# Kernel optimization log

Hardware: AMD Instinct MI355X
Metric: run time of the kernel (lower is better)

## Reference

```python
import jax, jax.numpy as jnp
import numpy as np

N_SAMPLES = 32768; N_FRAMES = 128; MODEL_DIM = 128; N_EVENTS = 16
N_BANDS = 64; RESOLUTION = 32; SR = 22050.0; WINDOW = 512; STEP = 256
DILATIONS = [1, 3, 9, 27, 1]

def conv1d(x, w, b, dilation=1):
    # x (B,C,T), w (O,I,K), 'same' padding
    k = w.shape[-1]; total = dilation * (k - 1)
    pad = (total // 2, total - total // 2)
    y = jax.lax.conv_general_dilated(x, w, (1,), [pad], rhs_dilation=(dilation,),
                                     dimension_numbers=('NCH', 'OIH', 'NCH'))
    return y + b[None, :, None]

def conv_transpose1d(x, w, b):
    # torch ConvTranspose1d(k=4, s=2, p=1): doubles length
    y = jax.lax.conv_general_dilated(x, w[..., ::-1], (1,), [(2, 2)], lhs_dilation=(2,),
                                     dimension_numbers=('NCH', 'OIH', 'NCH'))
    return y + b[None, :, None]

def example_norm(x):
    n = jnp.sqrt(jnp.sum(x * x, axis=(1, 2), keepdims=True))
    return x / (n + 1e-8)

def interp_linear(x, size):
    # F.interpolate(mode='linear', align_corners=False)
    T = x.shape[-1]
    c = jnp.clip((jnp.arange(size) + 0.5) * T / size - 0.5, 0.0, T - 1.0)
    i0 = jnp.floor(c).astype(jnp.int32)
    i1 = jnp.minimum(i0 + 1, T - 1)
    w = (c - i0).astype(x.dtype)
    return x[..., i0] * (1 - w) + x[..., i1] * w

def fft_convolve(a, b):
    n = a.shape[-1]
    pa = [(0, 0)] * (a.ndim - 1) + [(0, n)]
    pb = [(0, 0)] * (b.ndim - 1) + [(0, n)]
    spec = jnp.fft.rfft(jnp.pad(a, pa), norm='ortho') * jnp.fft.rfft(jnp.pad(b, pb), norm='ortho')
    return jnp.fft.irfft(spec, n=2 * n, norm='ortho')[..., :n]

def conv_up_nearest(z, lin_w, lin_b, up_w, up_b, out_w, out_b, start):
    h = (z @ lin_w.T + lin_b).reshape(-1, MODEL_DIM, start)
    for i in range(up_w.shape[0]):
        h = jnp.repeat(h, 2, axis=-1)
        h = jax.nn.leaky_relu(conv1d(h, up_w[i], up_b[i]), 0.2)
    return conv1d(h, out_w, out_b)

def conv_up_learned(z, lin_w, lin_b, up_w, up_b, out_w, out_b, start):
    h = (z @ lin_w.T + lin_b).reshape(-1, MODEL_DIM, start)
    for i in range(up_w.shape[0]):
        h = jax.nn.leaky_relu(conv_transpose1d(h, up_w[i], up_b[i]), 0.2)
    return conv1d(h, out_w, out_b)

def resonance_bank():
    # (n_bands, resolution, n_samples): per-band sinusoid * per-resolution frame-wise decay
    freqs = jnp.geomspace(20.0, SR * 0.45, N_BANDS)
    t = jnp.arange(N_SAMPLES, dtype=jnp.float32) / SR
    sines = jnp.sin(2.0 * np.pi * freqs[:, None] * t[None, :])
    decays = jnp.linspace(0.5, 0.9999, RESOLUTION)
    amp = decays[:, None] ** jnp.arange(N_FRAMES, dtype=jnp.float32)[None, :]
    amp = jnp.repeat(amp, N_SAMPLES // N_FRAMES, axis=-1)  # (res, N)
    return sines[:, None, :] * amp[None, :, :]

def _forward(x, noise, fb_w, reduce_w, reduce_b, dl_dw, dl_db, dl_pw, dl_pb,
             tt_w, tt_b, tr_w, tr_b,
             pos_lin_w, pos_lin_b, pos_up_w, pos_up_b, pos_out_w, pos_out_b,
             env_lin_w, env_lin_b, env_up_w, env_up_b, env_out_w, env_out_b,
             tfu_lin_w, tfu_lin_b, tfu_up_w, tfu_up_b, tfu_out_w, tfu_out_b):
    batch = x.shape[0]
    # filterbank conv + temporal pooling (avg pool 512/256) -> (B, 128, 128)
    h = jax.lax.conv_general_dilated(x, fb_w, (1,), [(256, 255)],
                                     dimension_numbers=('NCH', 'OIH', 'NCH'))
    h = jax.lax.reduce_window(h, 0.0, jax.lax.add, (1, 1, WINDOW), (1, 1, STEP),
                              [(0, 0), (0, 0), (STEP, STEP)]) / WINDOW
    h = example_norm(h[..., :N_FRAMES])
    # positional encoding: 1 + 16 sin + 16 cos = 33 channels
    p = jnp.linspace(-1.0, 1.0, N_FRAMES)
    bands = [p[None]]
    for i in range(16):
        f = p * (2.0 ** i) * np.pi
        bands.append(jnp.sin(f)[None]); bands.append(jnp.cos(f)[None])
    pos = jnp.broadcast_to(jnp.concatenate(bands, axis=0)[None], (batch, 33, N_FRAMES)).astype(x.dtype)
    h = jnp.concatenate([h, pos], axis=1)
    h = jnp.einsum('oc,bct->bot', reduce_w, h) + reduce_b[None, :, None]
    # dilated context stack with residuals
    for i, d in enumerate(DILATIONS):
        y = conv1d(h, dl_dw[i], dl_db[i], dilation=d)
        y = jnp.einsum('oc,bct->bot', dl_pw[i], y) + dl_pb[i][None, :, None]
        h = jax.nn.leaky_relu(h + y, 0.2)
    h = example_norm(h)
    # vectorwise top-k sparsity: keep 16 unit-normalized time-step vectors
    norms = jnp.sqrt(jnp.sum(h * h, axis=1))               # (B, T)
    hn = h / (norms[:, None, :] + 1e-8)
    _, idx = jax.lax.top_k(norms, N_EVENTS)                # (B, 16)
    encoded = jnp.take_along_axis(hn.transpose(0, 2, 1), idx[..., None], axis=1)  # (B,16,C)
    e = encoded.reshape(-1, MODEL_DIM)                     # (B*16, C)
    time = e @ tt_w.T + tt_b
    transfer = e @ tr_w.T + tr_b                           # VQ is passthrough
    # impulse placement: learned upsample -> softmax -> sparse comb
    pimp = conv_up_learned(time, pos_lin_w, pos_lin_b, pos_up_w, pos_up_b, pos_out_w, pos_out_b, 4).reshape(-1, 128)
    impulse = jnp.zeros((pimp.shape[0], N_SAMPLES), pimp.dtype).at[:, ::N_SAMPLES // 128].set(jax.nn.softmax(pimp, axis=-1))
    impulse = impulse.reshape(batch, N_EVENTS, N_SAMPLES)
    # segment generator: envelope * noise, transfer-function decode via FFT conv
    env = jax.nn.relu(conv_up_nearest(transfer, env_lin_w, env_lin_b, env_up_w, env_up_b, env_out_w, env_out_b, 4))  # (BE,1,256)
    orig_env = env
    envs = interp_linear(env, N_SAMPLES) * noise           # (BE,1,N)
    tfl = conv_up_nearest(transfer, tfu_lin_w, tfu_lin_b, tfu_up_w, tfu_up_b, tfu_out_w, tfu_out_b, 8)  # (BE,32,bands)
    tfl = tfl.transpose(0, 2, 1)                           # (BE,bands,res)
    sm = jax.nn.softmax(tfl, axis=-1)
    hard = jax.nn.one_hot(jnp.argmax(tfl, axis=-1), RESOLUTION, dtype=tfl.dtype)
    sel = sm + jax.lax.stop_gradient(hard - sm)            # straight-through hard select
    bank = resonance_bank().astype(x.dtype)
    tf_sig = jnp.einsum('ebr,brt->ebt', sel, bank)         # (BE,bands,N)
    final = jnp.mean(fft_convolve(envs, tf_sig), axis=1, keepdims=True)  # (BE,1,N)
    ev = fft_convolve(final.reshape(batch, N_EVENTS, N_SAMPLES), impulse)
    output = jnp.sum(ev, axis=1, keepdims=True)            # (B,1,N)
    return output, idx, encoded, orig_env.reshape(batch, N_EVENTS, -1), time, transfer

def setup_inputs() -> dict:
    key = jax.random.key(0)
    ks = jax.random.split(key, 32)
    r = lambda i, shape: jax.random.normal(ks[i], shape, dtype=jnp.float32) * 0.05
    B = 1
    return {
        'x': jax.random.normal(ks[0], (B, 1, N_SAMPLES), dtype=jnp.float32),
        'noise': jax.random.uniform(ks[1], (1, 1, N_SAMPLES), minval=-1.0, maxval=1.0, dtype=jnp.float32),
        'fb_w': r(2, (128, 1, 512)),
        'reduce_w': r(3, (128, 161)), 'reduce_b': r(4, (128,)),
        'dl_dw': r(5, (5, 128, 128, 3)), 'dl_db': r(6, (5, 128)),
        'dl_pw': r(7, (5, 128, 128)), 'dl_pb': r(8, (5, 128)),
        'tt_w': r(9, (128, 128)), 'tt_b': r(10, (128,)),
        'tr_w': r(11, (128, 128)), 'tr_b': r(12, (128,)),
        'pos_lin_w': r(13, (512, 128)), 'pos_lin_b': r(14, (512,)),
        'pos_up_w': r(15, (5, 128, 128, 4)), 'pos_up_b': r(16, (5, 128)),
        'pos_out_w': r(17, (1, 128, 3)), 'pos_out_b': r(18, (1,)),
        'env_lin_w': r(19, (512, 128)), 'env_lin_b': r(20, (512,)),
        'env_up_w': r(21, (6, 128, 128, 3)), 'env_up_b': r(22, (6, 128)),
        'env_out_w': r(23, (1, 128, 3)), 'env_out_b': r(24, (1,)),
        'tfu_lin_w': r(25, (1024, 128)), 'tfu_lin_b': r(26, (1024,)),
        'tfu_up_w': r(27, (3, 128, 128, 3)), 'tfu_up_b': r(28, (3, 128)),
        'tfu_out_w': r(29, (32, 128, 3)), 'tfu_out_b': r(30, (32,)),
    }

def reference(x, noise, fb_w, reduce_w, reduce_b, dl_dw, dl_db, dl_pw, dl_pb,
              tt_w, tt_b, tr_w, tr_b,
              pos_lin_w, pos_lin_b, pos_up_w, pos_up_b, pos_out_w, pos_out_b,
              env_lin_w, env_lin_b, env_up_w, env_up_b, env_out_w, env_out_b,
              tfu_lin_w, tfu_lin_b, tfu_up_w, tfu_up_b, tfu_out_w, tfu_out_b):
    return _forward(x, noise, fb_w, reduce_w, reduce_b, dl_dw, dl_db, dl_pw, dl_pb,
                    tt_w, tt_b, tr_w, tr_b,
                    pos_lin_w, pos_lin_b, pos_up_w, pos_up_b, pos_out_w, pos_out_b,
                    env_lin_w, env_lin_b, env_up_w, env_up_b, env_out_w, env_out_b,
                    tfu_lin_w, tfu_lin_b, tfu_up_w, tfu_up_b, tfu_out_w, tfu_out_b)
```

## Files before the change

kernel.cpp:

```cpp
#include <hip/hip_runtime.h>
#include <math.h>

#define NSAMP 32768
#define NFRM  128

static constexpr int S_OFF  = 0;
static constexpr int HP     = 32772;
static constexpr int NSQ    = HP + 16384;
static constexpr int HA     = NSQ + 16;
static constexpr int HB     = HA + 16384;
static constexpr int TFQ    = HA;
static constexpr int WC     = HB + 16384;
static constexpr int WBC    = WC + 245760;
static constexpr int EWS    = WBC + 640;
static constexpr int TIMEO  = EWS + 2048;
static constexpr int TRANSO = TIMEO + 2048;
static constexpr int PE     = TRANSO + 2048;
static constexpr int RSEL   = PE + 2048;
static constexpr int ENVO   = RSEL + 1024;
static constexpr int BUFA   = ENVO + 4096;
static constexpr int BUFB   = BUFA + 524288;
static constexpr int WT     = BUFB + 524288;
static constexpr int WT_POS = WT;
static constexpr int WT_ENV = WT + 327680;
static constexpr int WT_TFU = WT + 622592;
static constexpr int WT_TT  = WT + 770048;
static constexpr int WT_TR  = WT + 786432;
static constexpr int LT_POS = WT + 802816;
static constexpr int LT_ENV = WT + 868352;
static constexpr int LT_TFU = WT + 933888;
static constexpr int SINES  = WT + 1064960;
static constexpr int ENVS   = SINES + 2097152;
static constexpr int SLAB   = SINES;
static constexpr int CRB0   = ENVS + 524288;
static constexpr int CRB1   = CRB0 + 262656;
static constexpr int KB     = CRB1 + 262656;
static constexpr int PA     = KB + 278528;
static constexpr int PB     = PA + 262144;
static constexpr int TA     = PB + 262144;
static constexpr int TB     = TA + 131072;

static constexpr int O_IDX  = 32768;
static constexpr int O_ENC  = 32784;
static constexpr int O_ENV  = 34832;
static constexpr int O_TIME = 38928;
static constexpr int O_TR   = 40976;

typedef short bf16x8 __attribute__((ext_vector_type(8)));
typedef float f32x4  __attribute__((ext_vector_type(4)));
typedef float f32x16 __attribute__((ext_vector_type(16)));

static __device__ __forceinline__ unsigned short f2bf(float f){
  unsigned int u = __float_as_uint(f);
  unsigned int r = (u + 0x7FFFu + ((u >> 16) & 1u)) >> 16;
  return (unsigned short)r;
}

__global__ void k_setup(const float* __restrict__ x,
                        const float* __restrict__ posw, const float* __restrict__ envw,
                        const float* __restrict__ tfuw, const float* __restrict__ ttw,
                        const float* __restrict__ trw,  const float* __restrict__ lpw,
                        const float* __restrict__ lew,  const float* __restrict__ ltw,
                        const float* __restrict__ dw,   const float* __restrict__ db,
                        const float* __restrict__ pw,   const float* __restrict__ pb2,
                        float* __restrict__ ws){
  __shared__ float ps[1024];
  int b = blockIdx.x, tid = threadIdx.x;
  if (b == 0){
    float* S = ws + S_OFF;
    float v[32];
    const float4* x4 = (const float4*)(x + tid*32);
    float s = 0.f;
#pragma unroll
    for (int i=0;i<8;++i){
      float4 q = x4[i];
      v[4*i]=q.x; v[4*i+1]=q.y; v[4*i+2]=q.z; v[4*i+3]=q.w;
      s += q.x+q.y+q.z+q.w;
    }
    ps[tid] = s; __syncthreads();
    for (int ofs=1; ofs<1024; ofs<<=1){
      float add = (tid>=ofs)? ps[tid-ofs] : 0.f;
      __syncthreads();
      ps[tid] += add;
      __syncthreads();
    }
    float run = ps[tid] - s;
#pragma unroll
    for (int i=0;i<32;++i){ S[tid*32+i] = run; run += v[i]; }
    if (tid==1023) S[32768] = ps[1023];
  } else if (b < 1041){
    int i = (b-1)*1024 + tid;
    float v;
    if (i < 327680){
      int l = i>>16, r = i & 65535, o = r & 127, ck = r>>7, c = ck>>2, k = ck&3;
      v = posw[(l<<16) + (((o<<7)+c)<<2) + k];
    } else if (i < 622592){
      int i2 = i - 327680; int l = i2/49152, r = i2 - l*49152, o = r&127, ck = r>>7;
      int c = ck/3, k = ck - 3*c;
      v = envw[l*49152 + ((o<<7)+c)*3 + k];
    } else if (i < 770048){
      int i2 = i - 622592; int l = i2/49152, r = i2 - l*49152, o = r&127, ck = r>>7;
      int c = ck/3, k = ck - 3*c;
      v = tfuw[l*49152 + ((o<<7)+c)*3 + k];
    } else if (i < 786432){
      int i2 = i - 770048; int o = i2 & 127, c = i2 >> 7;
      v = ttw[(o<<7) + c];
    } else if (i < 802816){
      int i2 = i - 786432; int o = i2 & 127, c = i2 >> 7;
      v = trw[(o<<7) + c];
    } else if (i < 868352){
      int i2 = i - 802816; int s = i2 >> 14, k = (i2 >> 7) & 127, c = i2 & 127;
      v = lpw[(((c<<2)+s)<<7) + k];
    } else if (i < 933888){
      int i2 = i - 868352; int s = i2 >> 14, k = (i2 >> 7) & 127, c = i2 & 127;
      v = lew[(((c<<2)+s)<<7) + k];
    } else {
      int i2 = i - 933888; int s = i2 >> 14, k = (i2 >> 7) & 127, c = i2 & 127;
      v = ltw[(((c<<3)+s)<<7) + k];
    }
    ws[WT + i] = v;
  } else if (b < 1121){
    int idx = (b-1041)*1024 + tid;
    if (idx < 81920){
      int l = idx >> 14, r = idx & 16383, o = r >> 7, c = r & 127;
      float a0=0.f, a1=0.f, a2=0.f;
      for (int m=0;m<128;++m){
        float p = pw[(l*128 + o)*128 + m];
        const float* dp = dw + ((l*128 + m)*128 + c)*3;
        a0 += p*dp[0]; a1 += p*dp[1]; a2 += p*dp[2];
      }
      float* W = ws + WC + ((l*128 + o)*128 + c)*3;
      W[0]=a0; W[1]=a1; W[2]=a2;
      if (c==0){
        float bb = pb2[l*128 + o];
        for (int m=0;m<128;++m) bb += pw[(l*128 + o)*128 + m] * db[l*128 + m];
        ws[WBC + l*128 + o] = bb;
      }
    }
  } else if (b < 3169){
    int b2 = b - 1121;
    int band = b2 >> 5;
    int t = ((b2 & 31) << 10) + tid;
    if (tid == 0){
      float l0 = __fdiv_rn((float)log(20.0),   (float)log(10.0));
      float l1 = __fdiv_rn((float)log(9922.5), (float)log(10.0));
      float dl = __fdiv_rn(__fsub_rn(l1, l0), 63.0f);
      float lb = __fadd_rn(l0, __fmul_rn((float)band, dl));
      float freq = (float)pow(10.0, (double)lb);
      ps[0] = __fmul_rn((float)(2.0*M_PI), freq);
    }
    __syncthreads();
    float w = ps[0];
    float tn = __fdiv_rn((float)t, 22050.0f);
    ws[SINES + band*NSAMP + t] = sinf(__fmul_rn(w, tn));
  } else {
    int i = (b-3169)*1024 + tid;
    {
      int e = i >> 11, r = i & 2047;
      ((unsigned short*)(ws + KB))[e*34816 + r] = 0;
    }
    if (i < 16*128){
      int e = i >> 7, r = i & 127;
      if (r < 64) ((unsigned short*)(ws + CRB0))[e*32832 + (r==0 ? 0 : 32768 + r)] = 0;
      else        ((unsigned short*)(ws + CRB1))[e*32832 + 32768 + (r-64)] = 0;
    }
  }
}


__global__ void k_fbpool(const float* __restrict__ fbw, float* __restrict__ ws){
  const float* S = ws + S_OFF;
  int c = blockIdx.x >> 5, j0 = (blockIdx.x & 31) << 2;
  int jj = threadIdx.x >> 7, kk = threadIdx.x & 127;
  int j = j0 + jj;
  int i0 = max(0, 256*j - 256), i1 = min(32767, 256*j + 255);
  float acc = 0.f;
#pragma unroll
  for (int m=0;m<4;++m){
    int k = kk + (m<<7);
    int hi = min(max(i1 + k - 255, 0), 32768);
    int lo = min(max(i0 + k - 256, 0), 32768);
    acc += fbw[c*512 + k] * (S[hi] - S[lo]);
  }
  for (int o=32;o;o>>=1) acc += __shfl_down(acc, o);
  __shared__ float red[8];
  if ((threadIdx.x & 63) == 0) red[threadIdx.x>>6] = acc;
  __syncthreads();
  if (threadIdx.x < 4)
    ws[HP + c*128 + j0 + threadIdx.x] = (red[2*threadIdx.x] + red[2*threadIdx.x+1]) * (1.0f/512.0f);
}

__global__ void k_reduce(const float* __restrict__ rw, const float* __restrict__ rb,
                         float* __restrict__ ws){
  int o = blockIdx.x, t = threadIdx.x;
  const float* hp = ws + HP;
  float sq = 0.f;
  for (int i=t;i<16384;i+=128){ float v = hp[i]; sq += v*v; }
  for (int ofs=32;ofs;ofs>>=1) sq += __shfl_down(sq, ofs);
  __shared__ float rr2[2];
  if ((t & 63) == 0) rr2[t>>6] = sq;
  __syncthreads();
  float g = sqrtf(rr2[0] + rr2[1]) + 1e-8f;
  float acc = rb[o];
  for (int c=0;c<128;++c) acc += rw[o*161 + c] * __fdiv_rn(hp[c*128 + t], g);
  float delta = __fdiv_rn(2.0f, 127.0f);
  float p = __fadd_rn(-1.0f, __fmul_rn((float)t, delta));
  acc += rw[o*161 + 128] * p;
  float sc = 1.0f;
  const float PIF = (float)M_PI;
#pragma unroll
  for (int i=0;i<16;++i){
    float f = __fmul_rn(__fmul_rn(p, sc), PIF);
    acc += rw[o*161 + 129 + 2*i] * sinf(f);
    acc += rw[o*161 + 130 + 2*i] * cosf(f);
    sc = sc * 2.0f;
  }
  ws[HA + o*128 + t] = acc;
}

__global__ void k_dil(float* __restrict__ ws, int l, int d, int inoff, int outoff){
  __shared__ float xin[16384];
  __shared__ float pr[256];
  int o = blockIdx.x, tid = threadIdx.x;
  int t = tid & 127, half = tid >> 7;
  const float* in = ws + inoff;
  for (int idx=tid; idx<16384; idx+=256) xin[idx] = in[idx];
  __syncthreads();
  const float* Wo = ws + WC + (l*128 + o)*384 + half*192;
  float acc = (half == 0) ? (xin[o*128 + t] + ws[WBC + l*128 + o]) : 0.f;
  int cbase = half << 6;
  for (int c2=0;c2<64;++c2){
    int c = cbase + c2;
    float v0 = (t-d >= 0)  ? xin[c*128 + t - d] : 0.f;
    float v1 = xin[c*128 + t];
    float v2 = (t+d < 128) ? xin[c*128 + t + d] : 0.f;
    acc += Wo[c2*3]*v0 + Wo[c2*3+1]*v1 + Wo[c2*3+2]*v2;
  }
  pr[half*128 + t] = acc;
  __syncthreads();
  if (tid < 128){
    float a = pr[tid] + pr[128 + tid];
    ws[outoff + o*128 + tid] = a >= 0.f ? a : 0.2f*a;
  }
}

__global__ void k_topk(float* __restrict__ ws, float* __restrict__ out){
  const float* h = ws + HB;
  int tid = threadIdx.x;
  int g = tid >> 7, t = tid & 127;
  __shared__ float xs[16384];
  __shared__ float part[1024];
  __shared__ float nt[128], nt0[128], csh[128];
  __shared__ int idxs[16];
  __shared__ float gsh[1];
  __shared__ float wv[2]; __shared__ int wi[2];
  for (int idx=tid; idx<16384; idx+=1024){
    int c = idx >> 7, tt = idx & 127;
    xs[(c<<7) + ((tt+c)&127)] = h[idx];
  }
  __syncthreads();
  float p = 0.f;
  for (int c=g; c<128; c+=8){ float v = xs[(c<<7) + ((t+c)&127)]; p += v*v; }
  part[tid] = p;
  __syncthreads();
  if (tid < 128){
    float cs = 0.f;
#pragma unroll
    for (int gg=0; gg<8; ++gg) cs += part[(gg<<7) + tid];
    csh[tid] = cs;
  }
  __syncthreads();
  if (tid < 64){
    float s = csh[tid] + csh[tid+64];
    for (int o=32;o;o>>=1) s += __shfl_down(s, o);
    if (tid == 0) gsh[0] = sqrtf(s) + 1e-8f;
  }
  __syncthreads();
  float g2 = gsh[0];
  float p2 = 0.f;
  for (int c=g; c<128; c+=8){ float v = __fdiv_rn(xs[(c<<7) + ((t+c)&127)], g2); p2 += v*v; }
  part[tid] = p2;
  __syncthreads();
  if (tid < 128){
    float cs = 0.f;
#pragma unroll
    for (int gg=0; gg<8; ++gg) cs += part[(gg<<7) + tid];
    float ntv = sqrtf(cs);
    nt[tid] = ntv; nt0[tid] = ntv;
  }
  __syncthreads();
  for (int j=0;j<16;++j){
    if (tid < 128){
      float v = nt[t]; int bi = t;
      for (int o=32;o;o>>=1){
        float ov = __shfl_down(v, o); int oi = __shfl_down(bi, o);
        if (ov > v || (ov == v && oi < bi)){ v = ov; bi = oi; }
      }
      if ((t & 63) == 0){ wv[t>>6] = v; wi[t>>6] = bi; }
    }
    __syncthreads();
    if (tid == 0){
      int win = (wv[1] > wv[0] || (wv[1] == wv[0] && wi[1] < wi[0])) ? wi[1] : wi[0];
      idxs[j] = win; nt[win] = -3.0e38f;
    }
    __syncthreads();
  }
  if (tid < 16) out[O_IDX + tid] = (float)idxs[tid];
  for (int pos=tid; pos<2048; pos+=1024){
    int j = pos >> 7, ch = pos & 127;
    int ij = idxs[j];
    float hv = __fdiv_rn(xs[(ch<<7) + ((ij+ch)&127)], g2);
    float enc = __fdiv_rn(hv, nt0[ij] + 1e-8f);
    out[O_ENC + pos] = enc;
    ws[EWS + pos] = enc;
  }
}

__global__ void k_tt(float* __restrict__ ws, const float* __restrict__ ttb,
                     const float* __restrict__ trb, float* __restrict__ out){
  int kind = blockIdx.x >> 4, j = blockIdx.x & 15;
  int tid = threadIdx.x;
  int o = tid & 127, cg = tid >> 7;
  __shared__ float er[128];
  __shared__ float part[8][128];
  if (tid < 128) er[tid] = ws[EWS + j*128 + tid];
  __syncthreads();
  const float* Wt = ws + (kind ? WT_TR : WT_TT);
  float acc = 0.f;
  for (int c=cg; c<128; c+=8) acc += er[c] * Wt[c*128 + o];
  part[cg][o] = acc;
  __syncthreads();
  if (tid < 128){
    float a = kind ? trb[tid] : ttb[tid];
#pragma unroll
    for (int g=0; g<8; ++g) a += part[g][tid];
    out[(kind ? O_TR : O_TIME) + j*128 + tid] = a;
    ws[(kind ? TRANSO : TIMEO) + j*128 + tid] = a;
  }
}


__global__ void k_lin3(float* __restrict__ ws, const float* __restrict__ plb,
                       const float* __restrict__ elb, const float* __restrict__ tlb){
  int b = blockIdx.x, tid = threadIdx.x;
  int kg = tid >> 7, c = tid & 127;
  int e, s, start, ltoff, zoff, dst;
  const float* lb;
  if (b < 64){
    e = b >> 2; s = b & 3; start = 4; ltoff = LT_POS; zoff = TIMEO; dst = PA; lb = plb;
  } else if (b < 128){
    int b2 = b - 64; e = b2 >> 2; s = b2 & 3; start = 4; ltoff = LT_ENV; zoff = TRANSO; dst = BUFA; lb = elb;
  } else {
    int b2 = b - 128; e = b2 >> 3; s = b2 & 7; start = 8; ltoff = LT_TFU; zoff = TRANSO; dst = TA; lb = tlb;
  }
  __shared__ float z[128];
  __shared__ float part[8][128];
  if (tid < 128) z[tid] = ws[zoff + e*128 + tid];
  __syncthreads();
  const float* lt = ws + ltoff + (s << 14);
  float acc = 0.f;
  for (int k=kg; k<128; k+=8) acc += z[k] * lt[(k<<7) + c];
  part[kg][c] = acc;
  __syncthreads();
  if (tid < 128){
    float a = lb[tid*start + s];
#pragma unroll
    for (int g=0; g<8; ++g) a += part[g][tid];
    ws[dst + e*(start<<7) + (s<<7) + tid] = a;
  }
}

static __device__ __forceinline__ void convT8_dev(float* __restrict__ ws, const float* __restrict__ bias,
                                                  int srcoff, int dstoff, int wtoff, int Lin,
                                                  int e, int jt, float* xs, float* wl){
  int j0 = jt*8, o = threadIdx.x;
  int s_lo = (j0 >> 1) - 1;
  const float* in = ws + srcoff + e*Lin*128;
  for (int idx=o; idx<6*128; idx+=128){
    int si = idx >> 7, c = idx & 127, s = s_lo + si;
    xs[idx] = (s >= 0 && s < Lin) ? in[s*128 + c] : 0.f;
  }
  float acc[8];
#pragma unroll
  for (int jj=0;jj<8;++jj) acc[jj] = bias[o];
  const float* wt = ws + wtoff;
#pragma unroll 1
  for (int cb=0; cb<128; cb+=16){
    __syncthreads();
    for (int idx=o; idx<8192; idx+=128) wl[idx] = wt[(cb<<9) + idx];
    __syncthreads();
#pragma unroll
    for (int cc=0; cc<16; ++cc){
      int c = cb + cc;
      float w0 = wl[((cc<<2)+0)*128 + o];
      float w1 = wl[((cc<<2)+1)*128 + o];
      float w2 = wl[((cc<<2)+2)*128 + o];
      float w3 = wl[((cc<<2)+3)*128 + o];
      float xr[6];
#pragma unroll
      for (int s=0;s<6;++s) xr[s] = xs[(s<<7) + c];
#pragma unroll
      for (int jj=0;jj<8;++jj){
        if ((jj & 1) == 0){
          acc[jj] += xr[jj>>1]*w3 + xr[(jj>>1)+1]*w1;
        } else {
          acc[jj] += xr[(jj+1)>>1]*w2 + xr[((jj+1)>>1)+1]*w0;
        }
      }
    }
  }
  float* outp = ws + dstoff + e*(Lin*2)*128;
#pragma unroll
  for (int jj=0;jj<8;++jj){
    float v = acc[jj];
    outp[(j0+jj)*128 + o] = v >= 0.f ? v : 0.2f*v;
  }
}

static __device__ __forceinline__ void conv3up8_dev(float* __restrict__ ws, const float* __restrict__ bias,
                                                    int srcoff, int dstoff, int wtoff, int Lin,
                                                    int e, int jt, float* xs, float* wl){
  int j0 = jt*8, o = threadIdx.x;
  int fs = (j0 >> 1) - 1;
  const float* in = ws + srcoff + e*Lin*128;
  for (int idx=o; idx<6*128; idx+=128){
    int si = idx >> 7, c = idx & 127, s = fs + si;
    xs[idx] = (s >= 0 && s < Lin) ? in[s*128 + c] : 0.f;
  }
  float acc[8];
#pragma unroll
  for (int jj=0;jj<8;++jj) acc[jj] = bias[o];
  const float* wt = ws + wtoff;
#pragma unroll 1
  for (int cb=0; cb<128; cb+=16){
    __syncthreads();
    for (int idx=o; idx<6144; idx+=128) wl[idx] = wt[cb*384 + idx];
    __syncthreads();
#pragma unroll
    for (int cc=0; cc<16; ++cc){
      int c = cb + cc;
      float w0 = wl[(cc*3+0)*128 + o];
      float w1 = wl[(cc*3+1)*128 + o];
      float w2 = wl[(cc*3+2)*128 + o];
      float xr[6];
#pragma unroll
      for (int s=0;s<6;++s) xr[s] = xs[(s<<7) + c];
#pragma unroll
      for (int jj=0;jj<8;++jj){
        acc[jj] += xr[((jj-1)>>1)+1]*w0
                 + xr[((jj  )>>1)+1]*w1
                 + xr[((jj+1)>>1)+1]*w2;
      }
    }
  }
  float* outp = ws + dstoff + e*(Lin*2)*128;
#pragma unroll
  for (int jj=0;jj<8;++jj){
    float v = acc[jj];
    outp[(j0+jj)*128 + o] = v >= 0.f ? v : 0.2f*v;
  }
}

__global__ __launch_bounds__(128, 4)
void k_layer(float* __restrict__ ws, const float* __restrict__ pbias,
             const float* __restrict__ ebias, const float* __restrict__ tbias,
             int c1, int c2,
             int pLin, int pWt, int pBo, int pNJ, int pSrc, int pDst,
             int eLin, int eWt, int eBo, int eNJ, int eSrc, int eDst,
             int tLin, int tWt, int tBo, int tNJ, int tSrc, int tDst){
  __shared__ float xs[6*128];
  __shared__ float wl[8192];
  int b = blockIdx.x;
  if (b < c1){
    int e = b / pNJ, jt = b - e*pNJ;
    convT8_dev(ws, pbias + pBo, pSrc, pDst, pWt, pLin, e, jt, xs, wl);
  } else if (b < c2){
    int bl = b - c1; int e = bl / eNJ, jt = bl - e*eNJ;
    conv3up8_dev(ws, ebias + eBo, eSrc, eDst, eWt, eLin, e, jt, xs, wl);
  } else {
    int bl = b - c2; int e = bl / tNJ, jt = bl - e*tNJ;
    conv3up8_dev(ws, tbias + tBo, tSrc, tDst, tWt, tLin, e, jt, xs, wl);
  }
}

__global__ void k_outs(float* __restrict__ ws,
                       const float* __restrict__ pw, const float* __restrict__ pb,
                       const float* __restrict__ ew, const float* __restrict__ eb,
                       const float* __restrict__ tw, const float* __restrict__ tb_,
                       float* __restrict__ out){
  __shared__ float xs[16384];
  int b = blockIdx.x, tid = threadIdx.x;
  if (b < 16){
    int e = b;
    const float* in = ws + PB + e*16384;
    for (int idx=tid; idx<16384; idx+=512){
      int q = idx >> 7, c = idx & 127;
      xs[(q<<7) + ((c+q)&127)] = in[idx];
    }
    __syncthreads();
    int j = tid & 127, cg = tid >> 7;
    float acc = (cg == 0) ? pb[0] : 0.f;
    int cbase = cg << 5;
    for (int c2=0;c2<32;++c2){
      int c = cbase + c2;
#pragma unroll
      for (int k=0;k<3;++k){
        int q = j + k - 1;
        if (q >= 0 && q < 128) acc += xs[(q<<7) + ((c+q)&127)] * pw[c*3 + k];
      }
    }
    __syncthreads();
    xs[tid] = acc;
    __syncthreads();
    float a = 0.f;
    if (tid < 128) a = xs[tid] + xs[128+tid] + xs[256+tid] + xs[384+tid];
    __syncthreads();
    xs[tid] = (tid < 128) ? a : -3.0e38f;
    __syncthreads();
    for (int s=256; s>=1; s>>=1){ if (tid < s) xs[tid] = fmaxf(xs[tid], xs[tid+s]); __syncthreads(); }
    float m = xs[0];
    __syncthreads();
    float ex = (tid < 128) ? expf(__fsub_rn(a, m)) : 0.f;
    xs[tid] = ex;
    __syncthreads();
    for (int s=256; s>=1; s>>=1){ if (tid < s) xs[tid] += xs[tid+s]; __syncthreads(); }
    if (tid < 128) ws[PE + e*128 + tid] = __fdiv_rn(ex, xs[0]);
  } else if (b < 80){
    int idx2 = b - 16; int e = idx2 >> 2, b0 = (idx2 & 3) << 6;
    const float* in = ws + BUFA + e*32768;
    for (int idx=tid; idx<8448; idx+=512){
      int qs = idx >> 7, c = idx & 127, q = b0 - 1 + qs;
      xs[(qs<<7) + ((c+qs)&127)] = (q >= 0 && q < 256) ? in[q*128 + c] : 0.f;
    }
    __syncthreads();
    int part = tid >> 6, bb = tid & 63;
    float acc = (part == 0) ? eb[0] : 0.f;
    for (int c2=0;c2<16;++c2){
      int c = part*16 + c2;
#pragma unroll
      for (int k=0;k<3;++k){
        int qs = bb + k;
        acc += xs[(qs<<7) + ((c+qs)&127)] * ew[c*3 + k];
      }
    }
    xs[8448 + tid] = acc;
    __syncthreads();
    if (tid < 64){
      float a = 0.f;
#pragma unroll
      for (int g=0; g<8; ++g) a += xs[8448 + g*64 + tid];
      a = fmaxf(a, 0.f);
      out[O_ENV + e*256 + b0 + tid] = a;
      ws[ENVO + e*256 + b0 + tid] = a;
    }
  } else {
    int b2 = b - 80; int e = b2 >> 2, rg = b2 & 3;
    float* tws = xs + 8448;
    const float* in = ws + TB + e*8192;
    for (int idx=tid; idx<8448; idx+=512){
      int qs = idx >> 7, c = idx & 127, q = -1 + qs;
      xs[(qs<<7) + ((c+qs)&127)] = (q >= 0 && q < 64) ? in[q*128 + c] : 0.f;
    }
    for (int idx=tid; idx<3072; idx+=512) tws[idx] = tw[rg*3072 + idx];
    __syncthreads();
    int rl = tid >> 6, bb = tid & 63;
    int rr = rg*8 + rl;
    float acc = tb_[rr];
    for (int c=0;c<128;++c){
#pragma unroll
      for (int k=0;k<3;++k){
        int qs = bb + k;
        acc += xs[(qs<<7) + ((c+qs)&127)] * tws[rl*384 + c*3 + k];
      }
    }
    ws[TFQ + e*2048 + rr*64 + bb] = acc;
  }
}


__global__ void k_envK(float* __restrict__ ws, const float* __restrict__ noise){
  int b = blockIdx.x, tid = threadIdx.x;
  if (b < 2048){
    int e = b >> 7, F = b & 127;
    int t = (F << 8) + tid;
    __shared__ float ampl[64];
    if (tid < 64){
      const float* tf = ws + TFQ + e*2048;
      float best = tf[tid]; int bi = 0;
      for (int r=1;r<32;++r){ float v = tf[r*64 + tid]; if (v > best){ best = v; bi = r; } }
      float d = __fadd_rn(0.5f, __fmul_rn((float)bi, __fdiv_rn(__fsub_rn(0.9999f, 0.5f), 31.0f)));
      ampl[tid] = (float)pow((double)d, (double)F);
    }
    __syncthreads();
    float acc = 0.f;
    for (int band=0;band<64;++band) acc += ws[SINES + band*NSAMP + t] * ampl[band];
    ((unsigned short*)(ws + KB))[e*34816 + 2048 + t] = f2bf(acc * (1.0f/(64.0f*65536.0f)));
  } else {
    int idx = (b - 2048)*256 + tid;
    int e = idx >> 15, tau = idx & 32767;
    float cf = __fsub_rn(__fdiv_rn(__fmul_rn(__fadd_rn((float)tau, 0.5f), 256.0f), 32768.0f), 0.5f);
    float c = fminf(fmaxf(cf, 0.0f), 255.0f);
    int i0 = (int)floorf(c);
    int i1 = min(i0 + 1, 255);
    float w = __fsub_rn(c, (float)i0);
    float e0 = ws[ENVO + e*256 + i0], e1 = ws[ENVO + e*256 + i1];
    float val = __fadd_rn(__fmul_rn(e0, __fsub_rn(1.0f, w)), __fmul_rn(e1, w));
    ws[ENVS + e*NSAMP + tau] = val * noise[tau];
  }
}

__global__ void k_c(float* __restrict__ ws){
  int e = blockIdx.x >> 5, seg = blockIdx.x & 31;
  int t = (seg << 10) + threadIdx.x;
  __shared__ float pl[128];
  if (threadIdx.x < 128) pl[threadIdx.x] = ws[PE + e*128 + threadIdx.x];
  __syncthreads();
  const float* ev = ws + ENVS + e*NSAMP;
  int kub = min(127, (seg << 2) + 3);
  float acc = 0.f;
  for (int k=0;k<=kub;++k){
    int u = t - (k << 8);
    if (u >= 0) acc += pl[k] * ev[u];
  }
  unsigned short hv = f2bf(acc);
  ((unsigned short*)(ws + CRB0))[e*32832 + 32768 - t] = hv;
  ((unsigned short*)(ws + CRB1))[e*32832 + 32767 - t] = hv;
}

__global__ __launch_bounds__(256, 4)
void k_bigmfma(float* __restrict__ ws){
  int b = blockIdx.x;
  int w = threadIdx.x >> 6;
  int lane = threadIdx.x & 63;
  int e = b / 72;
  int r = b - e*72;
  int T2 = 0, cum = 0;
  while (cum + ((T2+2)>>1) <= r){ cum += (T2+2)>>1; T2++; }
  int qb = r - cum;
  int nseg = 2*(T2+1);
  int seg = qb*4 + w;
  int t0 = T2 << 11;
  int il = lane & 31, h = lane >> 5;
  __shared__ __align__(16) float pool[4096];
  unsigned short* ks = (unsigned short*)pool;
  int wmax = nseg - 1 - qb*4; if (wmax > 3) wmax = 3;
  int U0 = -1984 + (qb << 12);
  int kcnt = wmax*1024 + 3008;
  const unsigned short* Kp = (const unsigned short*)(ws + KB) + e*34816 + 2048;
  {
    const unsigned short* src = Kp + U0;
    for (int i = threadIdx.x*8; i < kcnt; i += 2048){
      f32x4 v = *(const f32x4*)(src + i);
      *(f32x4*)(ks + i + ((i>>6)<<3)) = v;
    }
  }
  __syncthreads();
  f32x16 acc0 = {}; f32x16 acc1 = {};
  if (seg < nseg){
    int u0 = -1984 + (seg << 10);
    const unsigned short* C0p = (const unsigned short*)(ws + CRB0) + e*32832;
    const unsigned short* C1p = (const unsigned short*)(ws + CRB1) + e*32832;
    int ku  = (u0 - U0) + (il << 6) + (h << 3);
    int bA0 = 32768 - t0 + u0 - (il << 1) + (h << 3);
    int bA1 = bA0 - 2;
#pragma unroll 2
    for (int q = 0; q < 64; ++q){
      union { f32x4 v; bf16x8 s; } a0u, a1u, bu;
      a0u.v = *(const f32x4*)(C0p + bA0);
      a1u.v = *(const f32x4*)(C1p + bA1);
      int pa = ku + ((ku>>6)<<3);
      bu.v  = *(const f32x4*)(ks + pa);
      acc0 = __builtin_amdgcn_mfma_f32_32x32x16_bf16(a0u.s, bu.s, acc0, 0, 0, 0);
      acc1 = __builtin_amdgcn_mfma_f32_32x32x16_bf16(a1u.s, bu.s, acc1, 0, 0, 0);
      bA0 += 16; bA1 += 16; ku += 16;
    }
  }
  __syncthreads();
  float* red = pool;
  int wl = w & 1;
  if (w < 2){
#pragma unroll
    for (int rr = 0; rr < 16; ++rr){
      int row = (rr & 3) + ((rr >> 2) << 3) + (h << 2);
      red[(wl<<11) + (row << 6) + il]      = acc0[rr];
      red[(wl<<11) + (row << 6) + 32 + il] = acc1[rr];
    }
  }
  __syncthreads();
  if (w >= 2){
#pragma unroll
    for (int rr = 0; rr < 16; ++rr){
      int row = (rr & 3) + ((rr >> 2) << 3) + (h << 2);
      red[(wl<<11) + (row << 6) + il]      += acc0[rr];
      red[(wl<<11) + (row << 6) + 32 + il] += acc1[rr];
    }
  }
  __syncthreads();
  float* slab = ws + SLAB + b*2048;
  int tid = threadIdx.x;
#pragma unroll
  for (int jj = 0; jj < 8; ++jj){
    int pos = tid*8 + jj;
    int il2 = pos >> 6, x = pos & 63;
    int idx = ((x >> 1) << 6) + ((x & 1) << 5) + il2;
    slab[pos] = red[idx] + red[2048 + idx];
  }
}

__global__ void k_final(const float* __restrict__ ws, float* __restrict__ out){
  int t = blockIdx.x*1024 + threadIdx.x;
  int T2 = t >> 11, pos = t & 2047;
  int cum = 0;
  for (int j=0;j<T2;++j) cum += (j+2)>>1;
  int nb = (T2+2)>>1;
  float s = 0.f;
  for (int e=0;e<16;++e){
    const float* sl = ws + SLAB + (e*72 + cum)*2048 + pos;
    for (int q=0;q<nb;++q) s += sl[q*2048];
  }
  out[t] = s;
}


extern "C" void kernel_launch(void* const* d_in, const int* in_sizes, int n_in,
                              void* d_out, int out_size, void* d_ws, size_t ws_size,
                              hipStream_t stream){
  const float* x         = (const float*)d_in[0];
  const float* noise     = (const float*)d_in[1];
  const float* fb_w      = (const float*)d_in[2];
  const float* reduce_w  = (const float*)d_in[3];
  const float* reduce_b  = (const float*)d_in[4];
  const float* dl_dw     = (const float*)d_in[5];
  const float* dl_db     = (const float*)d_in[6];
  const float* dl_pw     = (const float*)d_in[7];
  const float* dl_pb     = (const float*)d_in[8];
  const float* tt_w      = (const float*)d_in[9];
  const float* tt_b      = (const float*)d_in[10];
  const float* tr_w      = (const float*)d_in[11];
  const float* tr_b      = (const float*)d_in[12];
  const float* pos_lin_w = (const float*)d_in[13];
  const float* pos_lin_b = (const float*)d_in[14];
  const float* pos_up_w  = (const float*)d_in[15];
  const float* pos_up_b  = (const float*)d_in[16];
  const float* pos_out_w = (const float*)d_in[17];
  const float* pos_out_b = (const float*)d_in[18];
  const float* env_lin_w = (const float*)d_in[19];
  const float* env_lin_b = (const float*)d_in[20];
  const float* env_up_w  = (const float*)d_in[21];
  const float* env_up_b  = (const float*)d_in[22];
  const float* env_out_w = (const float*)d_in[23];
  const float* env_out_b = (const float*)d_in[24];
  const float* tfu_lin_w = (const float*)d_in[25];
  const float* tfu_lin_b = (const float*)d_in[26];
  const float* tfu_up_w  = (const float*)d_in[27];
  const float* tfu_up_b  = (const float*)d_in[28];
  const float* tfu_out_w = (const float*)d_in[29];
  const float* tfu_out_b = (const float*)d_in[30];
  float* out = (float*)d_out;
  float* ws  = (float*)d_ws;

  k_setup<<<3201, 1024, 0, stream>>>(x, pos_up_w, env_up_w, tfu_up_w, tt_w, tr_w,
                                     pos_lin_w, env_lin_w, tfu_lin_w,
                                     dl_dw, dl_db, dl_pw, dl_pb, ws);
  k_fbpool<<<4096, 512, 0, stream>>>(fb_w, ws);
  k_reduce<<<128, 128, 0, stream>>>(reduce_w, reduce_b, ws);
  const int DIL[5] = {1, 3, 9, 27, 1};
  int src = HA, dst = HB;
  for (int l=0;l<5;++l){
    k_dil<<<128, 256, 0, stream>>>(ws, l, DIL[l], src, dst);
    int tmp = src; src = dst; dst = tmp;
  }
  k_topk<<<1, 1024, 0, stream>>>(ws, out);
  k_tt<<<32, 1024, 0, stream>>>(ws, tt_b, tr_b, out);
  k_lin3<<<256, 1024, 0, stream>>>(ws, pos_lin_b, env_lin_b, tfu_lin_b);

  k_layer<<<64, 128, 0, stream>>>(ws, pos_up_b, env_up_b, tfu_up_b, 16, 32,
      4,  WT_POS + 0,      0,   1, PA,   PB,
      4,  WT_ENV + 0,      0,   1, BUFA, BUFB,
      8,  WT_TFU + 0,      0,   2, TA,   TB);
  k_layer<<<128, 128, 0, stream>>>(ws, pos_up_b, env_up_b, tfu_up_b, 32, 64,
      8,  WT_POS + 65536,  128, 2, PB,   PA,
      8,  WT_ENV + 49152,  128, 2, BUFB, BUFA,
      16, WT_TFU + 49152,  128, 4, TB,   TA);
  k_layer<<<256, 128, 0, stream>>>(ws, pos_up_b, env_up_b, tfu_up_b, 64, 128,
      16, WT_POS + 131072, 256, 4, PA,   PB,
      16, WT_ENV + 98304,  256, 4, BUFA, BUFB,
      32, WT_TFU + 98304,  256, 8, TA,   TB);
  k_layer<<<256, 128, 0, stream>>>(ws, pos_up_b, env_up_b, tfu_up_b, 128, 256,
      32, WT_POS + 196608, 384, 8, PB,   PA,
      32, WT_ENV + 147456, 384, 8, BUFB, BUFA,
      1,  0,               0,   1, 0,    0);
  k_layer<<<512, 128, 0, stream>>>(ws, pos_up_b, env_up_b, tfu_up_b, 256, 512,
      64, WT_POS + 262144, 512, 16, PA,   PB,
      64, WT_ENV + 196608, 512, 16, BUFA, BUFB,
      1,  0,               0,   1, 0,    0);
  k_layer<<<512, 128, 0, stream>>>(ws, pos_up_b, env_up_b, tfu_up_b, 0, 512,
      1,  0,               0,   1, 0,    0,
      128, WT_ENV + 245760, 640, 32, BUFB, BUFA,
      1,  0,               0,   1, 0,    0);

  k_outs<<<144, 512, 0, stream>>>(ws, pos_out_w, pos_out_b, env_out_w, env_out_b,
                                  tfu_out_w, tfu_out_b, out);

  k_envK<<<4096, 256, 0, stream>>>(ws, noise);
  k_c<<<512, 1024, 0, stream>>>(ws);
  k_bigmfma<<<1152, 256, 0, stream>>>(ws);
  k_final<<<32, 1024, 0, stream>>>(ws, out);
}
```

Baseline: 558.9 us.

## Split example norm into separate kernel and widen reduce channel parallelism

Moves the global L2 norm and division into a new 16-block kernel that writes the normalized pooled features to scratch, so the reduce kernel no longer recomputes the 16K-element sum of squares in each of its 128 blocks. The reduce kernel now uses 512 threads, splitting the 128-channel dot product across four channel groups, and caches the weight row in shared memory. This adds one kernel launch and a scratch round trip, and it reuses the PA buffer, which later layers also write to.

```diff
diff --git a/kernel.cpp b/kernel.cpp
--- a/kernel.cpp
+++ b/kernel.cpp
@@ -190,32 +190,52 @@
     ws[HP + c*128 + j0 + threadIdx.x] = (red[2*threadIdx.x] + red[2*threadIdx.x+1]) * (1.0f/512.0f);
 }
 
+__global__ void k_norm(float* __restrict__ ws){
+  __shared__ float red[1024];
+  int b = blockIdx.x, tid = threadIdx.x;
+  const float* hp = ws + HP;
+  float s = 0.f;
+  for (int i=tid; i<16384; i+=1024){ float v = hp[i]; s += v*v; }
+  red[tid] = s; __syncthreads();
+  for (int ofs=512; ofs>=1; ofs>>=1){ if (tid < ofs) red[tid] += red[tid+ofs]; __syncthreads(); }
+  float g = sqrtf(red[0]) + 1e-8f;
+  int i = b*1024 + tid;
+  ws[PA + i] = __fdiv_rn(hp[i], g);
+}
+
 __global__ void k_reduce(const float* __restrict__ rw, const float* __restrict__ rb,
                          float* __restrict__ ws){
-  int o = blockIdx.x, t = threadIdx.x;
-  const float* hp = ws + HP;
-  float sq = 0.f;
-  for (int i=t;i<16384;i+=128){ float v = hp[i]; sq += v*v; }
-  for (int ofs=32;ofs;ofs>>=1) sq += __shfl_down(sq, ofs);
-  __shared__ float rr2[2];
-  if ((t & 63) == 0) rr2[t>>6] = sq;
-  __syncthreads();
-  float g = sqrtf(rr2[0] + rr2[1]) + 1e-8f;
-  float acc = rb[o];
-  for (int c=0;c<128;++c) acc += rw[o*161 + c] * __fdiv_rn(hp[c*128 + t], g);
-  float delta = __fdiv_rn(2.0f, 127.0f);
-  float p = __fadd_rn(-1.0f, __fmul_rn((float)t, delta));
-  acc += rw[o*161 + 128] * p;
-  float sc = 1.0f;
-  const float PIF = (float)M_PI;
-#pragma unroll
-  for (int i=0;i<16;++i){
-    float f = __fmul_rn(__fmul_rn(p, sc), PIF);
-    acc += rw[o*161 + 129 + 2*i] * sinf(f);
-    acc += rw[o*161 + 130 + 2*i] * cosf(f);
-    sc = sc * 2.0f;
-  }
-  ws[HA + o*128 + t] = acc;
+  int o = blockIdx.x, tid = threadIdx.x;
+  int t = tid & 127, cg = tid >> 7;
+  __shared__ float wl[161];
+  __shared__ float pr[512];
+  const float* hpn = ws + PA;
+  if (tid < 161) wl[tid] = rw[o*161 + tid];
+  __syncthreads();
+  float acc = 0.f;
+  int cb = cg << 5;
+  for (int c2=0;c2<32;++c2){
+    int c = cb + c2;
+    acc += wl[c] * hpn[(c<<7) + t];
+  }
+  pr[tid] = acc;
+  __syncthreads();
+  if (tid < 128){
+    float a = rb[o] + pr[tid] + pr[128+tid] + pr[256+tid] + pr[384+tid];
+    float delta = __fdiv_rn(2.0f, 127.0f);
+    float p = __fadd_rn(-1.0f, __fmul_rn((float)tid, delta));
+    a += wl[128] * p;
+    float sc = 1.0f;
+    const float PIF = (float)M_PI;
+#pragma unroll
+    for (int i=0;i<16;++i){
+      float f = __fmul_rn(__fmul_rn(p, sc), PIF);
+      a += wl[129 + 2*i] * sinf(f);
+      a += wl[130 + 2*i] * cosf(f);
+      sc = sc * 2.0f;
+    }
+    ws[HA + o*128 + tid] = a;
+  }
 }
 
 __global__ void k_dil(float* __restrict__ ws, int l, int d, int inoff, int outoff){
@@ -763,7 +783,8 @@
                                      pos_lin_w, env_lin_w, tfu_lin_w,
                                      dl_dw, dl_db, dl_pw, dl_pb, ws);
   k_fbpool<<<4096, 512, 0, stream>>>(fb_w, ws);
-  k_reduce<<<128, 128, 0, stream>>>(reduce_w, reduce_b, ws);
+  k_norm<<<16, 1024, 0, stream>>>(ws);
+  k_reduce<<<128, 512, 0, stream>>>(reduce_w, reduce_b, ws);
   const int DIL[5] = {1, 3, 9, 27, 1};
   int src = HA, dst = HB;
   for (int l=0;l<5;++l){
```

Result: faster. 525.7 us (-5.9%).
